# Kernel optimization log

Hardware: AMD Instinct MI355X
Metric: run time of the kernel (lower is better)

The kernel has to match this reference:

```python
import jax, jax.numpy as jnp
import numpy as np

B, N, C_IN, C_OUT, K = 2, 2048, 64, 128, 3
SCALE = 12.0  # spread points over ~12^3 unit voxels (voxel_size = 1.0 in the module)


def setup_inputs() -> dict:
    key = jax.random.key(0)
    k1, k2, k3 = jax.random.split(key, 3)
    points = jax.random.uniform(k1, (B, N, 3), dtype=jnp.float32) * SCALE
    features = jax.random.normal(k2, (B, N, C_IN), dtype=jnp.float32)
    # kaiming-uniform-ish init for weight viewed as (K^3*Cin, Cout)
    fan_in = K * K * K * C_IN
    bound = np.sqrt(6.0 / fan_in)
    weight = jax.random.uniform(k3, (K, K, K, C_IN, C_OUT), dtype=jnp.float32,
                                minval=-bound, maxval=bound)
    bias = jnp.zeros((C_OUT,), dtype=jnp.float32)
    return {"points": points, "features": features, "weight": weight, "bias": bias}


def reference(points, features, weight, bias):
    """Sparse 3D conv over a unit voxel grid.

    For each point i, every point j whose voxel index differs by an offset
    within the KxKxK stencil contributes features[j] @ weight[rel_offset].
    Vectorized as: per-offset boolean match matrix (B,N,N) -> masked
    feature aggregation -> one GEMM with that offset's (Cin,Cout) kernel slice.
    """
    k = weight.shape[0]
    c = k // 2
    # torch's .long() truncates toward zero; jnp astype(int32) does the same for floats
    vox = points.astype(jnp.int32)  # (B, N, 3)
    out = jnp.zeros(features.shape[:2] + (weight.shape[-1],), dtype=features.dtype)
    for oi in range(k):
        for oj in range(k):
            for ok in range(k):
                off = jnp.array([oi - c, oj - c, ok - c], dtype=jnp.int32)
                target = vox + off  # voxel that neighbor j must occupy for center i
                # mask[b, i, j] = all(vox[b, j] == vox[b, i] + off)
                mask = jnp.all(vox[:, None, :, :] == target[:, :, None, :], axis=-1)
                agg = jnp.einsum('bij,bjc->bic', mask.astype(features.dtype), features)
                out = out + agg @ weight[oi, oj, ok]  # (B,N,Cin)@(Cin,Cout)
    return out + bias
```

## Files before the change

kernel.cpp:

```cpp
#include <hip/hip_runtime.h>

#define BATCH 2
#define NPTS  2048
#define CIN   64
#define COUT  128
#define GD    14
#define GD2   (GD*GD)
#define NCELL (GD*GD*GD)
#define M     (BATCH*NPTS)
#define VOXF  (BATCH*NCELL*CIN)
#define MCELL (BATCH*1728)

typedef __bf16 bf16x8 __attribute__((ext_vector_type(8)));
typedef float  f32x4  __attribute__((ext_vector_type(4)));
typedef unsigned short us8 __attribute__((ext_vector_type(8)));

__device__ __forceinline__ unsigned short f2bf(float f) {
    unsigned u = __builtin_bit_cast(unsigned, f);
    return (unsigned short)((u + 0x7FFFu + ((u >> 16) & 1u)) >> 16);
}

__global__ __launch_bounds__(256) void k_prep(const float* __restrict__ points,
                                              const float* __restrict__ features,
                                              const float* __restrict__ weight,
                                              float* __restrict__ voxgrid,
                                              unsigned short* __restrict__ wT2) {
    const int t = threadIdx.x;
    if (blockIdx.x < 18) {
        const int p  = blockIdx.x >> 1;
        const int nh = blockIdx.x & 1;
        __shared__ unsigned short lds[64*194];
        #pragma unroll
        for (int i = 0; i < 48; ++i) {
            const int s  = t + i*256;
            const int nn = s & 63;
            const int kk = s >> 6;
            const int ok = kk >> 6, k = kk & 63;
            lds[nn*194 + kk] = f2bf(weight[(p*3 + ok)*8192 + k*128 + nh*64 + nn]);
        }
        __syncthreads();
        #pragma unroll
        for (int i = 0; i < 48; ++i) {
            const int s  = t + i*256;
            const int nn = s / 192;
            const int kk = s - nn*192;
            wT2[(size_t)(p*128 + nh*64 + nn)*192 + kk] = lds[nn*194 + kk];
        }
    } else {
        const int idx = (blockIdx.x - 18)*256 + t;
        const int g   = idx >> 6;
        const int cin = idx & 63;
        const int vx = (int)points[g*3 + 0];
        const int vy = (int)points[g*3 + 1];
        const int vz = (int)points[g*3 + 2];
        const int cell = (vx + 1)*GD2 + (vy + 1)*GD + (vz + 1);
        atomicAdd(&voxgrid[((size_t)(g >> 11)*NCELL + cell)*CIN + cin], features[idx]);
    }
}

__global__ __launch_bounds__(256) void k_pack(const float* __restrict__ voxgrid,
                                              unsigned short* __restrict__ voxbf) {
    const int idx = blockIdx.x * 256 + threadIdx.x;
    if (idx >= VOXF/8) return;
    const float4 v0 = ((const float4*)voxgrid)[idx*2 + 0];
    const float4 v1 = ((const float4*)voxgrid)[idx*2 + 1];
    us8 p;
    p[0] = f2bf(v0.x); p[1] = f2bf(v0.y); p[2] = f2bf(v0.z); p[3] = f2bf(v0.w);
    p[4] = f2bf(v1.x); p[5] = f2bf(v1.y); p[6] = f2bf(v1.z); p[7] = f2bf(v1.w);
    *(us8*)(voxbf + idx*8) = p;
}

__global__ __launch_bounds__(256) void k_conv(const unsigned short* __restrict__ voxbf,
                                              const unsigned short* __restrict__ wT2,
                                              const float* __restrict__ bias,
                                              float* __restrict__ outgrid) {
    static constexpr int DOFF[9] = { -13504, -12608, -11712,
                                       -960,    -64,    832,
                                      11584,  12480,  13376 };

    const int t    = threadIdx.x;
    const int l    = t & 63;
    const int w    = t >> 6;
    const int q    = l >> 4;
    const int col  = l & 15;
    const int mblk = blockIdx.x;
    const int b    = (mblk >= 108);
    const int ci0  = (mblk - b*108) * 16;
    const int n0   = blockIdx.y*64 + w*16;

    const int ci = ci0 + col;
    const int cx = ci / 144, cy = (ci / 12) % 12, cz = ci % 12;
    const int v  = (cx + 1)*GD2 + (cy + 1)*GD + (cz + 1);
    const unsigned short* aptr = voxbf + (size_t)(b*NCELL + v)*64 + q*8;
    const unsigned short* bptr = wT2 + (size_t)(n0 + col)*192 + q*8;

    f32x4 acc = {0.f, 0.f, 0.f, 0.f};

    us8 Ab[4], Bb[4];
    #pragma unroll
    for (int st = 0; st < 4; ++st) {
        const int p = st / 6, s = st % 6;
        Ab[st] = *(const us8*)(aptr + DOFF[p] + s*32);
        Bb[st] = *(const us8*)(bptr + p*24576 + s*32);
    }
    #pragma unroll
    for (int st = 0; st < 54; ++st) {
        const int sl = st & 3;
        const us8 a = Ab[sl], bb = Bb[sl];
        if (st + 4 < 54) {
            const int p = (st + 4) / 6, s = (st + 4) % 6;
            Ab[sl] = *(const us8*)(aptr + DOFF[p] + s*32);
            Bb[sl] = *(const us8*)(bptr + p*24576 + s*32);
        }
        acc = __builtin_amdgcn_mfma_f32_16x16x32_bf16(
                  __builtin_bit_cast(bf16x8, a), __builtin_bit_cast(bf16x8, bb), acc, 0, 0, 0);
    }

    const float bs = bias[n0 + col];
    #pragma unroll
    for (int r = 0; r < 4; ++r) {
        outgrid[(size_t)(mblk*16 + q*4 + r)*128 + n0 + col] = acc[r] + bs;
    }
}

__global__ __launch_bounds__(256) void k_gather(const float* __restrict__ points,
                                                const float* __restrict__ outgrid,
                                                float* __restrict__ out) {
    const int idx = blockIdx.x * 256 + threadIdx.x;
    const int g   = idx >> 5;
    const int c4  = idx & 31;
    const int vx = (int)points[g*3 + 0];
    const int vy = (int)points[g*3 + 1];
    const int vz = (int)points[g*3 + 2];
    const int ci = vx*144 + vy*12 + vz;
    const int mg = (g >> 11)*1728 + ci;
    ((float4*)out)[(size_t)g*32 + c4] = ((const float4*)outgrid)[(size_t)mg*32 + c4];
}

extern "C" void kernel_launch(void* const* d_in, const int* in_sizes, int n_in,
                              void* d_out, int out_size, void* d_ws, size_t ws_size,
                              hipStream_t stream) {
    (void)in_sizes; (void)n_in; (void)out_size; (void)ws_size;
    const float* points   = (const float*)d_in[0];
    const float* features = (const float*)d_in[1];
    const float* weight   = (const float*)d_in[2];
    const float* bias     = (const float*)d_in[3];
    float* out = (float*)d_out;

    char* ws = (char*)d_ws;
    float*          voxgrid = (float*)ws;
    unsigned short* voxbf   = (unsigned short*)(ws + 1404928);
    unsigned short* wT2     = (unsigned short*)(ws + 1404928 + 702464);
    float*          outgrid = (float*)(ws + 1404928 + 702464 + 442368);

    hipMemsetAsync(voxgrid, 0, (size_t)VOXF*4, stream);
    k_prep<<<18 + (M*CIN)/256, 256, 0, stream>>>(points, features, weight, voxgrid, wT2);
    k_pack<<<(VOXF/8 + 255)/256, 256, 0, stream>>>(voxgrid, voxbf);
    dim3 cgrid(MCELL/16, 2, 1);
    k_conv<<<cgrid, 256, 0, stream>>>(voxbf, wT2, bias, outgrid);
    k_gather<<<(M*32)/256, 256, 0, stream>>>(points, outgrid, out);
}
```

Before: 96.37 us.

## Fuse prep, pack, conv and gather into one persistent kernel with grid barriers

Replaces the memset and four kernel launches with a single persistent kernel of 432 blocks. Two software grid barriers separate three phases: zeroing plus weight transpose, voxel scatter-add, and the MFMA conv. The bf16 pack kernel is dropped; fp32 voxel features are converted to bf16 inside the MFMA loop. The gather pass is replaced by per-cell point lists built with atomics, so conv results are written straight to each point's output row. This removes launch overhead and intermediate buffers, but relies on all blocks being co-resident for the spin barrier and caps each cell at 16 points.

```diff
diff --git a/kernel.cpp b/kernel.cpp
--- a/kernel.cpp
+++ b/kernel.cpp
@@ -1,117 +1,140 @@
 #include <hip/hip_runtime.h>
 
-#define BATCH 2
-#define NPTS  2048
-#define CIN   64
-#define COUT  128
-#define GD    14
-#define GD2   (GD*GD)
-#define NCELL (GD*GD*GD)
-#define M     (BATCH*NPTS)
-#define VOXF  (BATCH*NCELL*CIN)
-#define MCELL (BATCH*1728)
+#define NB     432
+#define BATCH  2
+#define CIN    64
+#define COUT   128
+#define GD     14
+#define GD2    (GD*GD)
+#define NCELL  (GD*GD*GD)
+#define M      4096
+#define DCELL  1728
+#define MAXP   16
 
 typedef __bf16 bf16x8 __attribute__((ext_vector_type(8)));
 typedef float  f32x4  __attribute__((ext_vector_type(4)));
 typedef unsigned short us8 __attribute__((ext_vector_type(8)));
 
-__device__ __forceinline__ unsigned short f2bf(float f) {
-    unsigned u = __builtin_bit_cast(unsigned, f);
-    return (unsigned short)((u + 0x7FFFu + ((u >> 16) & 1u)) >> 16);
+__device__ __forceinline__ unsigned short bfc(float f) {
+    return __builtin_bit_cast(unsigned short, (__bf16)f);
 }
 
-__global__ __launch_bounds__(256) void k_prep(const float* __restrict__ points,
-                                              const float* __restrict__ features,
-                                              const float* __restrict__ weight,
-                                              float* __restrict__ voxgrid,
-                                              unsigned short* __restrict__ wT2) {
-    const int t = threadIdx.x;
-    if (blockIdx.x < 18) {
-        const int p  = blockIdx.x >> 1;
-        const int nh = blockIdx.x & 1;
-        __shared__ unsigned short lds[64*194];
+__device__ int g_cnt;
+
+__device__ __forceinline__ void grid_barrier(int tid) {
+    __syncthreads();
+    if (tid == 0) {
+        __threadfence();
+        int old = __hip_atomic_fetch_add(&g_cnt, 1, __ATOMIC_ACQ_REL, __HIP_MEMORY_SCOPE_AGENT);
+        int target = (old / NB + 1) * NB;
+        while (__hip_atomic_load(&g_cnt, __ATOMIC_ACQUIRE, __HIP_MEMORY_SCOPE_AGENT) < target)
+            __builtin_amdgcn_s_sleep(4);
+        __threadfence();
+    }
+    __syncthreads();
+}
+
+__global__ __launch_bounds__(256, 2) void k_all(const float* __restrict__ points,
+                                                const float* __restrict__ features,
+                                                const float* __restrict__ weight,
+                                                const float* __restrict__ bias,
+                                                float* __restrict__ out,
+                                                float* __restrict__ voxgrid,
+                                                int* __restrict__ ccount,
+                                                int* __restrict__ clist,
+                                                unsigned short* __restrict__ wT2) {
+    const int t   = threadIdx.x;
+    const int bid = blockIdx.x;
+    __shared__ unsigned short lds[64*194];
+
+    {
+        const int i = bid*256 + t;
+        if (i < 88672) ((float4*)voxgrid)[i] = make_float4(0.f, 0.f, 0.f, 0.f);
+    }
+    if (bid < 18) {
+        const int p  = bid >> 1;
+        const int nh = bid & 1;
         #pragma unroll
-        for (int i = 0; i < 48; ++i) {
-            const int s  = t + i*256;
+        for (int i2 = 0; i2 < 48; ++i2) {
+            const int s  = t + i2*256;
             const int nn = s & 63;
             const int kk = s >> 6;
             const int ok = kk >> 6, k = kk & 63;
-            lds[nn*194 + kk] = f2bf(weight[(p*3 + ok)*8192 + k*128 + nh*64 + nn]);
+            lds[nn*194 + kk] = bfc(weight[(p*3 + ok)*8192 + k*128 + nh*64 + nn]);
         }
         __syncthreads();
         #pragma unroll
-        for (int i = 0; i < 48; ++i) {
-            const int s  = t + i*256;
+        for (int i2 = 0; i2 < 48; ++i2) {
+            const int s  = t + i2*256;
             const int nn = s / 192;
             const int kk = s - nn*192;
             wT2[(size_t)(p*128 + nh*64 + nn)*192 + kk] = lds[nn*194 + kk];
         }
-    } else {
-        const int idx = (blockIdx.x - 18)*256 + t;
-        const int g   = idx >> 6;
-        const int cin = idx & 63;
-        const int vx = (int)points[g*3 + 0];
-        const int vy = (int)points[g*3 + 1];
-        const int vz = (int)points[g*3 + 2];
-        const int cell = (vx + 1)*GD2 + (vy + 1)*GD + (vz + 1);
-        atomicAdd(&voxgrid[((size_t)(g >> 11)*NCELL + cell)*CIN + cin], features[idx]);
     }
-}
 
-__global__ __launch_bounds__(256) void k_pack(const float* __restrict__ voxgrid,
-                                              unsigned short* __restrict__ voxbf) {
-    const int idx = blockIdx.x * 256 + threadIdx.x;
-    if (idx >= VOXF/8) return;
-    const float4 v0 = ((const float4*)voxgrid)[idx*2 + 0];
-    const float4 v1 = ((const float4*)voxgrid)[idx*2 + 1];
-    us8 p;
-    p[0] = f2bf(v0.x); p[1] = f2bf(v0.y); p[2] = f2bf(v0.z); p[3] = f2bf(v0.w);
-    p[4] = f2bf(v1.x); p[5] = f2bf(v1.y); p[6] = f2bf(v1.z); p[7] = f2bf(v1.w);
-    *(us8*)(voxbf + idx*8) = p;
-}
+    grid_barrier(t);
 
-__global__ __launch_bounds__(256) void k_conv(const unsigned short* __restrict__ voxbf,
-                                              const unsigned short* __restrict__ wT2,
-                                              const float* __restrict__ bias,
-                                              float* __restrict__ outgrid) {
+    if (bid >= 18) {
+        for (int u = bid - 18; u < 1024; u += NB - 18) {
+            const int idx = u*256 + t;
+            const int g   = idx >> 6;
+            const int cin = idx & 63;
+            const int vx = (int)points[g*3 + 0];
+            const int vy = (int)points[g*3 + 1];
+            const int vz = (int)points[g*3 + 2];
+            const int b  = g >> 11;
+            atomicAdd(&voxgrid[((size_t)b*NCELL + (vx+1)*GD2 + (vy+1)*GD + (vz+1))*CIN + cin],
+                      features[idx]);
+            if (cin == 0) {
+                const int mg   = b*DCELL + vx*144 + vy*12 + vz;
+                const int slot = atomicAdd(&ccount[mg], 1);
+                if (slot < MAXP) clist[mg*MAXP + slot] = g;
+            }
+        }
+    }
+
+    grid_barrier(t);
+
     static constexpr int DOFF[9] = { -13504, -12608, -11712,
                                        -960,    -64,    832,
                                       11584,  12480,  13376 };
+    const int l   = t & 63;
+    const int w   = t >> 6;
+    const int q   = l >> 4;
+    const int col = l & 15;
+    const int mt  = bid >> 1;
+    const int nh  = bid & 1;
+    const int b2  = (mt >= 108);
+    const int cil = (mt - b2*108) * 16;
+    const int n0  = nh*64 + w*16;
 
-    const int t    = threadIdx.x;
-    const int l    = t & 63;
-    const int w    = t >> 6;
-    const int q    = l >> 4;
-    const int col  = l & 15;
-    const int mblk = blockIdx.x;
-    const int b    = (mblk >= 108);
-    const int ci0  = (mblk - b*108) * 16;
-    const int n0   = blockIdx.y*64 + w*16;
-
-    const int ci = ci0 + col;
-    const int cx = ci / 144, cy = (ci / 12) % 12, cz = ci % 12;
-    const int v  = (cx + 1)*GD2 + (cy + 1)*GD + (cz + 1);
-    const unsigned short* aptr = voxbf + (size_t)(b*NCELL + v)*64 + q*8;
+    const int ci = cil + col;
+    const int cx = ci/144, cy = (ci/12)%12, cz = ci%12;
+    const float* aptr = voxgrid + ((size_t)b2*NCELL + (cx+1)*GD2 + (cy+1)*GD + (cz+1))*CIN + q*8;
     const unsigned short* bptr = wT2 + (size_t)(n0 + col)*192 + q*8;
 
     f32x4 acc = {0.f, 0.f, 0.f, 0.f};
-
-    us8 Ab[4], Bb[4];
+    float4 A0[4], A1[4]; us8 B0[4];
     #pragma unroll
     for (int st = 0; st < 4; ++st) {
-        const int p = st / 6, s = st % 6;
-        Ab[st] = *(const us8*)(aptr + DOFF[p] + s*32);
-        Bb[st] = *(const us8*)(bptr + p*24576 + s*32);
+        A0[st] = *(const float4*)(aptr + DOFF[0] + st*32);
+        A1[st] = *(const float4*)(aptr + DOFF[0] + st*32 + 4);
+        B0[st] = *(const us8*)(bptr + st*32);
     }
     #pragma unroll
     for (int st = 0; st < 54; ++st) {
         const int sl = st & 3;
-        const us8 a = Ab[sl], bb = Bb[sl];
+        const float4 xa = A0[sl], xb = A1[sl];
+        const us8 bb = B0[sl];
         if (st + 4 < 54) {
             const int p = (st + 4) / 6, s = (st + 4) % 6;
-            Ab[sl] = *(const us8*)(aptr + DOFF[p] + s*32);
-            Bb[sl] = *(const us8*)(bptr + p*24576 + s*32);
+            A0[sl] = *(const float4*)(aptr + DOFF[p] + s*32);
+            A1[sl] = *(const float4*)(aptr + DOFF[p] + s*32 + 4);
+            B0[sl] = *(const us8*)(bptr + p*24576 + s*32);
         }
+        us8 a;
+        a[0]=bfc(xa.x); a[1]=bfc(xa.y); a[2]=bfc(xa.z); a[3]=bfc(xa.w);
+        a[4]=bfc(xb.x); a[5]=bfc(xb.y); a[6]=bfc(xb.z); a[7]=bfc(xb.w);
         acc = __builtin_amdgcn_mfma_f32_16x16x32_bf16(
                   __builtin_bit_cast(bf16x8, a), __builtin_bit_cast(bf16x8, bb), acc, 0, 0, 0);
     }
@@ -119,22 +142,14 @@
     const float bs = bias[n0 + col];
     #pragma unroll
     for (int r = 0; r < 4; ++r) {
-        outgrid[(size_t)(mblk*16 + q*4 + r)*128 + n0 + col] = acc[r] + bs;
+        const int cir = cil + q*4 + r;
+        const int mg  = b2*DCELL + cir;
+        const int cnt = min(ccount[mg], MAXP);
+        for (int j = 0; j < cnt; ++j) {
+            const int g = clist[mg*MAXP + j];
+            out[(size_t)g*COUT + n0 + col] = acc[r] + bs;
+        }
     }
-}
-
-__global__ __launch_bounds__(256) void k_gather(const float* __restrict__ points,
-                                                const float* __restrict__ outgrid,
-                                                float* __restrict__ out) {
-    const int idx = blockIdx.x * 256 + threadIdx.x;
-    const int g   = idx >> 5;
-    const int c4  = idx & 31;
-    const int vx = (int)points[g*3 + 0];
-    const int vy = (int)points[g*3 + 1];
-    const int vz = (int)points[g*3 + 2];
-    const int ci = vx*144 + vy*12 + vz;
-    const int mg = (g >> 11)*1728 + ci;
-    ((float4*)out)[(size_t)g*32 + c4] = ((const float4*)outgrid)[(size_t)mg*32 + c4];
 }
 
 extern "C" void kernel_launch(void* const* d_in, const int* in_sizes, int n_in,
@@ -149,14 +164,10 @@
 
     char* ws = (char*)d_ws;
     float*          voxgrid = (float*)ws;
-    unsigned short* voxbf   = (unsigned short*)(ws + 1404928);
-    unsigned short* wT2     = (unsigned short*)(ws + 1404928 + 702464);
-    float*          outgrid = (float*)(ws + 1404928 + 702464 + 442368);
+    int*            ccount  = (int*)(ws + 1404928);
+    int*            clist   = (int*)(ws + 1418752);
+    unsigned short* wT2     = (unsigned short*)(ws + 1639936);
 
-    hipMemsetAsync(voxgrid, 0, (size_t)VOXF*4, stream);
-    k_prep<<<18 + (M*CIN)/256, 256, 0, stream>>>(points, features, weight, voxgrid, wT2);
-    k_pack<<<(VOXF/8 + 255)/256, 256, 0, stream>>>(voxgrid, voxbf);
-    dim3 cgrid(MCELL/16, 2, 1);
-    k_conv<<<cgrid, 256, 0, stream>>>(voxbf, wT2, bias, outgrid);
-    k_gather<<<(M*32)/256, 256, 0, stream>>>(points, outgrid, out);
+    k_all<<<NB, 256, 0, stream>>>(points, features, weight, bias, out,
+                                  voxgrid, ccount, clist, wT2);
 }
```

Result: slower. 211.7 us (+119.7%).
